# Performance work log

Hardware: AMD Instinct MI355X
Metric: run time of the kernel (lower is better)

Reference implementation:

```python
import jax, jax.numpy as jnp
import numpy as np
import math

D_MODEL = 768
NUM_HEADS = 12


def setup_inputs() -> dict:
    key = jax.random.key(0)
    ks = jax.random.split(key, 5)
    B, S, D = 2, 2048, D_MODEL
    scale = 1.0 / math.sqrt(D)
    x = jax.random.normal(ks[0], (B, S, D), dtype=jnp.float32)
    Wq = jax.random.normal(ks[1], (D, D), dtype=jnp.float32) * scale
    Wk = jax.random.normal(ks[2], (D, D), dtype=jnp.float32) * scale
    Wv = jax.random.normal(ks[3], (D, D), dtype=jnp.float32) * scale
    Wo = jax.random.normal(ks[4], (D, D), dtype=jnp.float32) * scale
    return {"x": x, "Wq": Wq, "Wk": Wk, "Wv": Wv, "Wo": Wo}


def _mhsa(x, Wq, Wk, Wv, Wo):
    B, S, D = x.shape
    H = NUM_HEADS
    hd = D // H
    # Linear(in, out) with weight [out, in]: y = x @ W^T
    q = x @ Wq.T
    k = x @ Wk.T
    v = x @ Wv.T
    # [B, S, H, hd] -> [B, H, S, hd]
    q = q.reshape(B, S, H, hd).transpose(0, 2, 1, 3)
    k = k.reshape(B, S, H, hd).transpose(0, 2, 1, 3)
    v = v.reshape(B, S, H, hd).transpose(0, 2, 1, 3)
    scores = jnp.einsum("bhqd,bhkd->bhqk", q, k) / jnp.sqrt(jnp.float32(hd))
    causal = jnp.tril(jnp.ones((S, S), dtype=bool))  # True where allowed
    scores = jnp.where(causal, scores, -jnp.inf)
    probs = jax.nn.softmax(scores, axis=-1)
    o = jnp.einsum("bhqk,bhkd->bhqd", probs, v)
    o = o.transpose(0, 2, 1, 3).reshape(B, S, D)
    return o @ Wo.T


def reference(x, Wq, Wk, Wv, Wo):
    return _mhsa(x, Wq, Wk, Wv, Wo)
```

## Files before the change

kernel.cpp:

```cpp
#include <hip/hip_runtime.h>
#include <math.h>

#define NHEAD 12
#define HD    64
#define SEQ   2048
#define BATCH 2
#define DM    768

typedef unsigned short u16;
typedef __attribute__((ext_vector_type(8))) short bf16x8;
typedef __attribute__((ext_vector_type(8))) unsigned short u16x8;
typedef __attribute__((ext_vector_type(4))) float f32x4;

__device__ __forceinline__ u16 f2bf(float f) {
    unsigned u = __builtin_bit_cast(unsigned, f);
    return (u16)((u + 0x7fffu + ((u >> 16) & 1u)) >> 16);
}
__device__ __forceinline__ bf16x8 as_bf16x8(uint4 v) { return __builtin_bit_cast(bf16x8, v); }
__device__ __forceinline__ u16x8  as_u16x8(uint4 v)  { return __builtin_bit_cast(u16x8, v); }
__device__ __forceinline__ f32x4 mfma16(bf16x8 a, bf16x8 b, f32x4 c) {
    return __builtin_amdgcn_mfma_f32_16x16x32_bf16(a, b, c, 0, 0, 0);
}

__global__ void cvt4(const float* __restrict__ s, u16* __restrict__ d, int n4) {
    int i = blockIdx.x * blockDim.x + threadIdx.x;
    if (i < n4) {
        float4 v = ((const float4*)s)[i];
        ushort4 o;
        o.x = f2bf(v.x); o.y = f2bf(v.y); o.z = f2bf(v.z); o.w = f2bf(v.w);
        ((ushort4*)d)[i] = o;
    }
}

__global__ void cvt4w(const float* __restrict__ s0, const float* __restrict__ s1,
                      const float* __restrict__ s2, const float* __restrict__ s3,
                      u16* __restrict__ d0, u16* __restrict__ d1,
                      u16* __restrict__ d2, u16* __restrict__ d3, int n4) {
    const float* s = blockIdx.y == 0 ? s0 : blockIdx.y == 1 ? s1 : blockIdx.y == 2 ? s2 : s3;
    u16*         d = blockIdx.y == 0 ? d0 : blockIdx.y == 1 ? d1 : blockIdx.y == 2 ? d2 : d3;
    int i = blockIdx.x * blockDim.x + threadIdx.x;
    if (i < n4) {
        float4 v = ((const float4*)s)[i];
        ushort4 o;
        o.x = f2bf(v.x); o.y = f2bf(v.y); o.z = f2bf(v.z); o.w = f2bf(v.w);
        ((ushort4*)d)[i] = o;
    }
}

__global__ __launch_bounds__(256)
void qkv_mfma(const u16* __restrict__ X,
              const u16* __restrict__ Wq, const u16* __restrict__ Wk,
              const u16* __restrict__ Wv,
              u16* __restrict__ Q, u16* __restrict__ K, u16* __restrict__ V)
{
    const u16* W = blockIdx.z == 0 ? Wq : blockIdx.z == 1 ? Wk : Wv;
    u16*       Y = blockIdx.z == 0 ? Q  : blockIdx.z == 1 ? K  : V;
    const int m0 = blockIdx.x * 128, n0 = blockIdx.y * 128;

    __shared__ __align__(16) u16 As[128 * 40];
    __shared__ __align__(16) u16 Bs[128 * 40];

    const int tid = threadIdx.x;
    const int w = tid >> 6, l = tid & 63, lg = l >> 4, lr = l & 15;
    const int wr = w >> 1, wc = w & 1;
    const int srow = tid >> 1, sh = tid & 1;

    const u16* ga = X + (size_t)(m0 + srow) * DM + sh * 16;
    const u16* gb = W + (size_t)(n0 + srow) * DM + sh * 16;
    const int sidx = srow * 40 + sh * 16;

    f32x4 acc[4][4];
    #pragma unroll
    for (int i = 0; i < 4; ++i)
        #pragma unroll
        for (int j = 0; j < 4; ++j) acc[i][j] = (f32x4){0.f, 0.f, 0.f, 0.f};

    for (int k0 = 0; k0 < DM; k0 += 32) {
        uint4 a0 = *(const uint4*)(ga + k0);
        uint4 a1 = *(const uint4*)(ga + k0 + 8);
        uint4 b0 = *(const uint4*)(gb + k0);
        uint4 b1 = *(const uint4*)(gb + k0 + 8);
        __syncthreads();
        *(uint4*)&As[sidx] = a0; *(uint4*)&As[sidx + 8] = a1;
        *(uint4*)&Bs[sidx] = b0; *(uint4*)&Bs[sidx + 8] = b1;
        __syncthreads();
        bf16x8 af[4], bfr[4];
        #pragma unroll
        for (int i = 0; i < 4; ++i) {
            af[i]  = as_bf16x8(*(const uint4*)&As[(wr * 64 + i * 16 + lr) * 40 + lg * 8]);
            bfr[i] = as_bf16x8(*(const uint4*)&Bs[(wc * 64 + i * 16 + lr) * 40 + lg * 8]);
        }
        __builtin_amdgcn_s_setprio(1);
        #pragma unroll
        for (int i = 0; i < 4; ++i)
            #pragma unroll
            for (int j = 0; j < 4; ++j)
                acc[i][j] = mfma16(af[i], bfr[j], acc[i][j]);
        __builtin_amdgcn_s_setprio(0);
    }

    #pragma unroll
    for (int i = 0; i < 4; ++i) {
        const int mb = m0 + wr * 64 + i * 16 + lg * 4;
        #pragma unroll
        for (int j = 0; j < 4; ++j) {
            const int n = n0 + wc * 64 + j * 16 + lr;
            const int h = n >> 6, dc = n & 63;
            #pragma unroll
            for (int r = 0; r < 4; ++r) {
                const int m = mb + r;
                const int b = m >> 11, s2 = m & 2047;
                Y[(((size_t)b * NHEAD + h) * SEQ + s2) * HD + dc] = f2bf(acc[i][j][r]);
            }
        }
    }
}

__global__ __launch_bounds__(256)
void attn_mfma(const u16* __restrict__ Qg, const u16* __restrict__ Kg,
               const u16* __restrict__ Vg, u16* __restrict__ Og)
{
    const int q0 = (31 - blockIdx.x) * 64;
    const int bh = blockIdx.y;
    const int kend = q0 >> 6;
    const size_t base = (size_t)bh * SEQ * HD;
    const u16* Qb = Qg + base;
    const u16* Kb = Kg + base;
    const u16* Vb = Vg + base;
    u16*       Ob = Og + base;

    __shared__ __align__(16) u16 Ks[64 * 64];
    __shared__ __align__(16) u16 Vt[64 * 64];
    __shared__ __align__(16) u16 Ps[4 * 16 * 64];

    const int tid = threadIdx.x;
    const int w = tid >> 6, l = tid & 63, lg = l >> 4, lr = l & 15;

    const int srow = w * 16 + (l >> 2);
    const int c0   = (l & 3) * 16;

    const int qrow = q0 + w * 16 + lr;
    bf16x8 qf[2];
    #pragma unroll
    for (int kh = 0; kh < 2; ++kh)
        qf[kh] = as_bf16x8(*(const uint4*)(Qb + (size_t)qrow * HD + kh * 32 + lg * 8));

    float ms[4], ls[4];
    f32x4 ov[4];
    #pragma unroll
    for (int r = 0; r < 4; ++r) { ms[r] = -INFINITY; ls[r] = 0.f; }
    #pragma unroll
    for (int dj = 0; dj < 4; ++dj) ov[dj] = (f32x4){0.f, 0.f, 0.f, 0.f};

    for (int kt = 0; kt <= kend; ++kt) {
        const int k0 = kt * 64;

        const u16* kp = Kb + (size_t)(k0 + srow) * HD + c0;
        const u16* vp = Vb + (size_t)(k0 + srow) * HD + c0;
        uint4 kq0 = *(const uint4*)(kp);
        uint4 kq1 = *(const uint4*)(kp + 8);
        uint4 vq0 = *(const uint4*)(vp);
        uint4 vq1 = *(const uint4*)(vp + 8);

        __syncthreads();
        {
            const int sw = (srow & 7) << 4;
            *(uint4*)&Ks[srow * 64 + (((c0 * 2) ^ sw) >> 1)]        = kq0;
            *(uint4*)&Ks[srow * 64 + ((((c0 + 8) * 2) ^ sw) >> 1)]  = kq1;
        }
        #pragma unroll
        for (int h = 0; h < 2; ++h) {
            u16x8 vv = as_u16x8(h ? vq1 : vq0);
            #pragma unroll
            for (int e = 0; e < 8; ++e) {
                const int d  = c0 + h * 8 + e;
                const int cs = (d & 7) ^ ((d >> 3) & 7);
                Vt[d * 64 + (((srow * 2) ^ (cs << 4)) >> 1)] = vv[e];
            }
        }
        __syncthreads();

        f32x4 sc[4];
        #pragma unroll
        for (int nj = 0; nj < 4; ++nj) sc[nj] = (f32x4){0.f, 0.f, 0.f, 0.f};
        __builtin_amdgcn_s_setprio(1);
        #pragma unroll
        for (int kh = 0; kh < 2; ++kh) {
            #pragma unroll
            for (int nj = 0; nj < 4; ++nj) {
                const int s  = nj * 16 + lr;
                const int cb = kh * 64 + lg * 16;
                bf16x8 kf = as_bf16x8(*(const uint4*)&Ks[s * 64 + ((cb ^ ((s & 7) << 4)) >> 1)]);
                sc[nj] = mfma16(qf[kh], kf, sc[nj]);
            }
        }
        __builtin_amdgcn_s_setprio(0);

        const bool lastt = (kt == kend);
        #pragma unroll
        for (int nj = 0; nj < 4; ++nj) {
            const int kk = k0 + nj * 16 + lr;
            #pragma unroll
            for (int r = 0; r < 4; ++r) {
                float v = sc[nj][r] * 0.125f;
                if (lastt && kk > (q0 + w * 16 + lg * 4 + r)) v = -INFINITY;
                sc[nj][r] = v;
            }
        }

        float fac[4];
        #pragma unroll
        for (int r = 0; r < 4; ++r) {
            float rm = fmaxf(fmaxf(sc[0][r], sc[1][r]), fmaxf(sc[2][r], sc[3][r]));
            rm = fmaxf(rm, __shfl_xor(rm, 1));
            rm = fmaxf(rm, __shfl_xor(rm, 2));
            rm = fmaxf(rm, __shfl_xor(rm, 4));
            rm = fmaxf(rm, __shfl_xor(rm, 8));
            const float mo = ms[r];
            const float mn = fmaxf(mo, rm);
            const float f  = __expf(mo - mn);
            ms[r] = mn; fac[r] = f;
            float rs = 0.f;
            #pragma unroll
            for (int nj = 0; nj < 4; ++nj) {
                const float pv = __expf(sc[nj][r] - mn);
                sc[nj][r] = pv;
                rs += pv;
            }
            rs += __shfl_xor(rs, 1); rs += __shfl_xor(rs, 2);
            rs += __shfl_xor(rs, 4); rs += __shfl_xor(rs, 8);
            ls[r] = ls[r] * f + rs;
        }

        #pragma unroll
        for (int dj = 0; dj < 4; ++dj)
            #pragma unroll
            for (int r = 0; r < 4; ++r)
                ov[dj][r] *= fac[r];
        #pragma unroll
        for (int nj = 0; nj < 4; ++nj)
            #pragma unroll
            for (int r = 0; r < 4; ++r) {
                const int row = lg * 4 + r, col = nj * 16 + lr;
                Ps[w * 1024 + row * 64 + (((col * 2) ^ ((row & 7) << 4)) >> 1)] = f2bf(sc[nj][r]);
            }

        __builtin_amdgcn_s_setprio(1);
        #pragma unroll
        for (int ks = 0; ks < 2; ++ks) {
            const int cb = ks * 64 + lg * 16;
            bf16x8 pa = as_bf16x8(*(const uint4*)&Ps[w * 1024 + lr * 64 + ((cb ^ ((lr & 7) << 4)) >> 1)]);
            #pragma unroll
            for (int dj = 0; dj < 4; ++dj) {
                const int d  = dj * 16 + lr;
                const int cs = (d & 7) ^ ((d >> 3) & 7);
                bf16x8 vf = as_bf16x8(*(const uint4*)&Vt[d * 64 + ((cb ^ (cs << 4)) >> 1)]);
                ov[dj] = mfma16(pa, vf, ov[dj]);
            }
        }
        __builtin_amdgcn_s_setprio(0);
    }

    #pragma unroll
    for (int r = 0; r < 4; ++r) {
        const float inv = 1.0f / ls[r];
        const int row = q0 + w * 16 + lg * 4 + r;
        #pragma unroll
        for (int dj = 0; dj < 4; ++dj)
            Ob[(size_t)row * HD + dj * 16 + lr] = f2bf(ov[dj][r] * inv);
    }
}

__global__ __launch_bounds__(256)
void proj_mfma(const u16* __restrict__ O, const u16* __restrict__ Wo,
               float* __restrict__ out)
{
    const int m0 = blockIdx.x * 128, n0 = blockIdx.y * 128;

    __shared__ __align__(16) u16 As[128 * 40];
    __shared__ __align__(16) u16 Bs[128 * 40];

    const int tid = threadIdx.x;
    const int w = tid >> 6, l = tid & 63, lg = l >> 4, lr = l & 15;
    const int wr = w >> 1, wc = w & 1;
    const int srow = tid >> 1, sh = tid & 1;

    const int m = m0 + srow;
    const int b = m >> 11, s2 = m & 2047;
    const u16* gb = Wo + (size_t)(n0 + srow) * DM + sh * 16;
    const int sidx = srow * 40 + sh * 16;

    f32x4 acc[4][4];
    #pragma unroll
    for (int i = 0; i < 4; ++i)
        #pragma unroll
        for (int j = 0; j < 4; ++j) acc[i][j] = (f32x4){0.f, 0.f, 0.f, 0.f};

    for (int k0 = 0; k0 < DM; k0 += 32) {
        const int kk = k0 + sh * 16;
        const u16* ga = O + (((size_t)b * NHEAD + (kk >> 6)) * SEQ + s2) * HD + (kk & 63);
        uint4 a0 = *(const uint4*)(ga);
        uint4 a1 = *(const uint4*)(ga + 8);
        uint4 b0 = *(const uint4*)(gb + k0);
        uint4 b1 = *(const uint4*)(gb + k0 + 8);
        __syncthreads();
        *(uint4*)&As[sidx] = a0; *(uint4*)&As[sidx + 8] = a1;
        *(uint4*)&Bs[sidx] = b0; *(uint4*)&Bs[sidx + 8] = b1;
        __syncthreads();
        bf16x8 af[4], bfr[4];
        #pragma unroll
        for (int i = 0; i < 4; ++i) {
            af[i]  = as_bf16x8(*(const uint4*)&As[(wr * 64 + i * 16 + lr) * 40 + lg * 8]);
            bfr[i] = as_bf16x8(*(const uint4*)&Bs[(wc * 64 + i * 16 + lr) * 40 + lg * 8]);
        }
        __builtin_amdgcn_s_setprio(1);
        #pragma unroll
        for (int i = 0; i < 4; ++i)
            #pragma unroll
            for (int j = 0; j < 4; ++j)
                acc[i][j] = mfma16(af[i], bfr[j], acc[i][j]);
        __builtin_amdgcn_s_setprio(0);
    }

    #pragma unroll
    for (int i = 0; i < 4; ++i) {
        const int mb = m0 + wr * 64 + i * 16 + lg * 4;
        #pragma unroll
        for (int j = 0; j < 4; ++j) {
            const int n = n0 + wc * 64 + j * 16 + lr;
            #pragma unroll
            for (int r = 0; r < 4; ++r)
                out[(size_t)(mb + r) * DM + n] = acc[i][j][r];
        }
    }
}

extern "C" void kernel_launch(void* const* d_in, const int* in_sizes, int n_in,
                              void* d_out, int out_size, void* d_ws, size_t ws_size,
                              hipStream_t stream)
{
    const float* x  = (const float*)d_in[0];
    const float* Wq = (const float*)d_in[1];
    const float* Wk = (const float*)d_in[2];
    const float* Wv = (const float*)d_in[3];
    const float* Wo = (const float*)d_in[4];
    float* out = (float*)d_out;

    const size_t nx = (size_t)BATCH * SEQ * DM;
    const size_t nw = (size_t)DM * DM;
    const size_t nh = (size_t)BATCH * NHEAD * SEQ * HD;

    u16* xb  = (u16*)d_ws;
    u16* wqb = xb  + nx;
    u16* wkb = wqb + nw;
    u16* wvb = wkb + nw;
    u16* wob = wvb + nw;
    u16* Qb  = wob + nw;
    u16* Kb  = Qb  + nh;
    u16* Vb  = Kb  + nh;
    u16* Ob  = Vb  + nh;

    cvt4<<<(int)(nx / 4 / 256), 256, 0, stream>>>(x, xb, (int)(nx / 4));
    dim3 gw((unsigned)(nw / 4 / 256), 4);
    cvt4w<<<gw, 256, 0, stream>>>(Wq, Wk, Wv, Wo, wqb, wkb, wvb, wob, (int)(nw / 4));

    dim3 g1(BATCH * SEQ / 128, DM / 128, 3);
    qkv_mfma<<<g1, 256, 0, stream>>>(xb, wqb, wkb, wvb, Qb, Kb, Vb);

    dim3 g2(32, BATCH * NHEAD);
    attn_mfma<<<g2, 256, 0, stream>>>(Qb, Kb, Vb, Ob);

    dim3 g3(BATCH * SEQ / 128, DM / 128);
    proj_mfma<<<g3, 256, 0, stream>>>(Ob, wob, out);
}
```

Baseline: 216.5 us.

## Transpose QK^T MFMA to keep P in registers, add lazy softmax rescale

The attention kernel now computes S^T by swapping MFMA operands, so each lane holds one query row's scores. This lets P be packed to bf16 in registers and fed straight into the PV MFMA, removing the Ps shared-memory round trip and most cross-lane reductions. The 1/sqrt(hd) scale is folded into the Q projection epilogue. Rescaling of the running max is skipped unless some row's max grows by more than 8, and per-row factors are redistributed with ds_bpermute. V fragments are now read as two 8-byte LDS loads to match the permuted key order, which may add bank conflicts or extra instructions.

```diff
diff --git a/kernel.cpp b/kernel.cpp
--- a/kernel.cpp
+++ b/kernel.cpp
@@ -55,6 +55,7 @@
 {
     const u16* W = blockIdx.z == 0 ? Wq : blockIdx.z == 1 ? Wk : Wv;
     u16*       Y = blockIdx.z == 0 ? Q  : blockIdx.z == 1 ? K  : V;
+    const float osc = (blockIdx.z == 0) ? 0.125f : 1.0f;
     const int m0 = blockIdx.x * 128, n0 = blockIdx.y * 128;
 
     __shared__ __align__(16) u16 As[128 * 40];
@@ -110,7 +111,7 @@
             for (int r = 0; r < 4; ++r) {
                 const int m = mb + r;
                 const int b = m >> 11, s2 = m & 2047;
-                Y[(((size_t)b * NHEAD + h) * SEQ + s2) * HD + dc] = f2bf(acc[i][j][r]);
+                Y[(((size_t)b * NHEAD + h) * SEQ + s2) * HD + dc] = f2bf(acc[i][j][r] * osc);
             }
         }
     }
@@ -131,7 +132,6 @@
 
     __shared__ __align__(16) u16 Ks[64 * 64];
     __shared__ __align__(16) u16 Vt[64 * 64];
-    __shared__ __align__(16) u16 Ps[4 * 16 * 64];
 
     const int tid = threadIdx.x;
     const int w = tid >> 6, l = tid & 63, lg = l >> 4, lr = l & 15;
@@ -145,10 +145,8 @@
     for (int kh = 0; kh < 2; ++kh)
         qf[kh] = as_bf16x8(*(const uint4*)(Qb + (size_t)qrow * HD + kh * 32 + lg * 8));
 
-    float ms[4], ls[4];
+    float ms = -INFINITY, lsum = 0.f;
     f32x4 ov[4];
-    #pragma unroll
-    for (int r = 0; r < 4; ++r) { ms[r] = -INFINITY; ls[r] = 0.f; }
     #pragma unroll
     for (int dj = 0; dj < 4; ++dj) ov[dj] = (f32x4){0.f, 0.f, 0.f, 0.f};
 
@@ -191,79 +189,91 @@
                 const int s  = nj * 16 + lr;
                 const int cb = kh * 64 + lg * 16;
                 bf16x8 kf = as_bf16x8(*(const uint4*)&Ks[s * 64 + ((cb ^ ((s & 7) << 4)) >> 1)]);
-                sc[nj] = mfma16(qf[kh], kf, sc[nj]);
+                sc[nj] = mfma16(kf, qf[kh], sc[nj]);
             }
         }
         __builtin_amdgcn_s_setprio(0);
 
-        const bool lastt = (kt == kend);
+        if (kt == kend) {
+            #pragma unroll
+            for (int nj = 0; nj < 4; ++nj)
+                #pragma unroll
+                for (int r = 0; r < 4; ++r) {
+                    const int key = k0 + nj * 16 + lg * 4 + r;
+                    if (key > qrow) sc[nj][r] = -INFINITY;
+                }
+        }
+
+        float pm = sc[0][0];
+        #pragma unroll
+        for (int nj = 0; nj < 4; ++nj)
+            #pragma unroll
+            for (int r = 0; r < 4; ++r) pm = fmaxf(pm, sc[nj][r]);
+        pm = fmaxf(pm, __shfl_xor(pm, 16));
+        pm = fmaxf(pm, __shfl_xor(pm, 32));
+
+        if (!__all(pm <= ms + 8.f)) {
+            const float mn  = fmaxf(ms, pm);
+            const float fac = __expf(ms - mn);
+            ms = mn;
+            lsum *= fac;
+            const int fi = __builtin_bit_cast(int, fac);
+            #pragma unroll
+            for (int r = 0; r < 4; ++r) {
+                const float fr = __builtin_bit_cast(float,
+                    __builtin_amdgcn_ds_bpermute((lg * 4 + r) * 4, fi));
+                #pragma unroll
+                for (int dj = 0; dj < 4; ++dj) ov[dj][r] *= fr;
+            }
+        }
+
+        float rs = 0.f;
+        #pragma unroll
+        for (int nj = 0; nj < 4; ++nj)
+            #pragma unroll
+            for (int r = 0; r < 4; ++r) {
+                const float p = __expf(sc[nj][r] - ms);
+                sc[nj][r] = p;
+                rs += p;
+            }
+        rs += __shfl_xor(rs, 16);
+        rs += __shfl_xor(rs, 32);
+        lsum += rs;
+
+        unsigned pw[4][2];
         #pragma unroll
         for (int nj = 0; nj < 4; ++nj) {
-            const int kk = k0 + nj * 16 + lr;
-            #pragma unroll
-            for (int r = 0; r < 4; ++r) {
-                float v = sc[nj][r] * 0.125f;
-                if (lastt && kk > (q0 + w * 16 + lg * 4 + r)) v = -INFINITY;
-                sc[nj][r] = v;
-            }
-        }
-
-        float fac[4];
-        #pragma unroll
-        for (int r = 0; r < 4; ++r) {
-            float rm = fmaxf(fmaxf(sc[0][r], sc[1][r]), fmaxf(sc[2][r], sc[3][r]));
-            rm = fmaxf(rm, __shfl_xor(rm, 1));
-            rm = fmaxf(rm, __shfl_xor(rm, 2));
-            rm = fmaxf(rm, __shfl_xor(rm, 4));
-            rm = fmaxf(rm, __shfl_xor(rm, 8));
-            const float mo = ms[r];
-            const float mn = fmaxf(mo, rm);
-            const float f  = __expf(mo - mn);
-            ms[r] = mn; fac[r] = f;
-            float rs = 0.f;
-            #pragma unroll
-            for (int nj = 0; nj < 4; ++nj) {
-                const float pv = __expf(sc[nj][r] - mn);
-                sc[nj][r] = pv;
-                rs += pv;
-            }
-            rs += __shfl_xor(rs, 1); rs += __shfl_xor(rs, 2);
-            rs += __shfl_xor(rs, 4); rs += __shfl_xor(rs, 8);
-            ls[r] = ls[r] * f + rs;
-        }
-
-        #pragma unroll
-        for (int dj = 0; dj < 4; ++dj)
-            #pragma unroll
-            for (int r = 0; r < 4; ++r)
-                ov[dj][r] *= fac[r];
-        #pragma unroll
-        for (int nj = 0; nj < 4; ++nj)
-            #pragma unroll
-            for (int r = 0; r < 4; ++r) {
-                const int row = lg * 4 + r, col = nj * 16 + lr;
-                Ps[w * 1024 + row * 64 + (((col * 2) ^ ((row & 7) << 4)) >> 1)] = f2bf(sc[nj][r]);
-            }
+            asm("v_cvt_pk_bf16_f32 %0, %1, %2" : "=v"(pw[nj][0]) : "v"(sc[nj][0]), "v"(sc[nj][1]));
+            asm("v_cvt_pk_bf16_f32 %0, %1, %2" : "=v"(pw[nj][1]) : "v"(sc[nj][2]), "v"(sc[nj][3]));
+        }
 
         __builtin_amdgcn_s_setprio(1);
         #pragma unroll
         for (int ks = 0; ks < 2; ++ks) {
-            const int cb = ks * 64 + lg * 16;
-            bf16x8 pa = as_bf16x8(*(const uint4*)&Ps[w * 1024 + lr * 64 + ((cb ^ ((lr & 7) << 4)) >> 1)]);
+            uint4 pa4;
+            pa4.x = pw[2 * ks][0]; pa4.y = pw[2 * ks][1];
+            pa4.z = pw[2 * ks + 1][0]; pa4.w = pw[2 * ks + 1][1];
+            const bf16x8 pa = as_bf16x8(pa4);
+            const int b0 = 64 * ks + 8 * lg;
             #pragma unroll
             for (int dj = 0; dj < 4; ++dj) {
                 const int d  = dj * 16 + lr;
                 const int cs = (d & 7) ^ ((d >> 3) & 7);
-                bf16x8 vf = as_bf16x8(*(const uint4*)&Vt[d * 64 + ((cb ^ (cs << 4)) >> 1)]);
-                ov[dj] = mfma16(pa, vf, ov[dj]);
+                const uint2 v0 = *(const uint2*)&Vt[d * 64 + ((b0 ^ (cs << 4)) >> 1)];
+                const uint2 v1 = *(const uint2*)&Vt[d * 64 + (((b0 + 32) ^ (cs << 4)) >> 1)];
+                uint4 vv; vv.x = v0.x; vv.y = v0.y; vv.z = v1.x; vv.w = v1.y;
+                ov[dj] = mfma16(pa, as_bf16x8(vv), ov[dj]);
             }
         }
         __builtin_amdgcn_s_setprio(0);
     }
 
+    const int li = __builtin_bit_cast(int, lsum);
     #pragma unroll
     for (int r = 0; r < 4; ++r) {
-        const float inv = 1.0f / ls[r];
+        const float lrow = __builtin_bit_cast(float,
+            __builtin_amdgcn_ds_bpermute((lg * 4 + r) * 4, li));
+        const float inv = 1.0f / lrow;
         const int row = q0 + w * 16 + lg * 4 + r;
         #pragma unroll
         for (int dj = 0; dj < 4; ++dj)
```

New measurement: 209.5 us. 1.03x faster.
